# Kernel tuning notes

Hardware: AMD Instinct MI355X
Metric: run time of the kernel (lower is better)

Reference implementation:

```python
import math
import jax, jax.numpy as jnp
import numpy as np
from jax import lax


def _p_n(num_param):
    # Fixed per-kernel sampling grid (torch _get_p_n), row-major over a
    # base_int-wide grid with a partial last row if num_param isn't square.
    base = round(math.sqrt(num_param))
    row = num_param // base
    mod = num_param % base
    xs = np.repeat(np.arange(row), base)
    ys = np.tile(np.arange(base), row)
    if mod > 0:
        xs = np.concatenate([xs, np.full(mod, row)])
        ys = np.concatenate([ys, np.arange(mod)])
    return jnp.asarray(np.concatenate([xs, ys]), jnp.float32)  # [2N]


def _gather_xq(x, q, N):
    # x: [b,c,H,W]; q: [b,h,w,2N] int32 -> [b,c,h,w,N]
    b, c, H, W = x.shape
    h, w = q.shape[1:3]
    idx = q[..., :N] * W + q[..., N:]               # [b,h,w,N]
    xf = x.reshape(b, c, H * W)
    out = jnp.take_along_axis(xf, idx.reshape(b, 1, h * w * N), axis=2)
    return out.reshape(b, c, h, w, N)


def ldconv_forward(x, w_p, b_p, w_conv, num_param, stride):
    b, c, H, W = x.shape
    N = num_param
    dn = ('NCHW', 'OIHW', 'NCHW')
    # offset conv: 3x3, pad 1, stride
    offset = lax.conv_general_dilated(x, w_p, (stride, stride),
                                      [(1, 1), (1, 1)], dimension_numbers=dn)
    offset = offset + b_p[None, :, None, None]      # [b,2N,h,w]
    h, w = offset.shape[2], offset.shape[3]

    p_n = _p_n(N).reshape(1, 2 * N, 1, 1)
    p0x = jnp.broadcast_to((jnp.arange(h, dtype=jnp.float32) * stride)[:, None], (h, w))
    p0y = jnp.broadcast_to((jnp.arange(w, dtype=jnp.float32) * stride)[None, :], (h, w))
    p_0 = jnp.concatenate([jnp.broadcast_to(p0x, (1, N, h, w)),
                           jnp.broadcast_to(p0y, (1, N, h, w))], axis=1)

    p = p_0 + p_n + offset                          # [b,2N,h,w]
    p = jnp.transpose(p, (0, 2, 3, 1))              # [b,h,w,2N]

    q_lt = jnp.floor(lax.stop_gradient(p))
    q_rb = q_lt + 1.0
    clampH = lambda v: jnp.clip(v, 0, H - 1)
    clampW = lambda v: jnp.clip(v, 0, W - 1)
    q_lt = jnp.concatenate([clampH(q_lt[..., :N]), clampW(q_lt[..., N:])], -1).astype(jnp.int32)
    q_rb = jnp.concatenate([clampH(q_rb[..., :N]), clampW(q_rb[..., N:])], -1).astype(jnp.int32)
    q_lb = jnp.concatenate([q_lt[..., :N], q_rb[..., N:]], -1)
    q_rt = jnp.concatenate([q_rb[..., :N], q_lt[..., N:]], -1)

    p = jnp.concatenate([clampH(p[..., :N]), clampW(p[..., N:])], -1)

    px, py = p[..., :N], p[..., N:]
    f = jnp.float32
    g_lt = (1 + (q_lt[..., :N].astype(f) - px)) * (1 + (q_lt[..., N:].astype(f) - py))
    g_rb = (1 - (q_rb[..., :N].astype(f) - px)) * (1 - (q_rb[..., N:].astype(f) - py))
    g_lb = (1 + (q_lb[..., :N].astype(f) - px)) * (1 - (q_lb[..., N:].astype(f) - py))
    g_rt = (1 - (q_rt[..., :N].astype(f) - px)) * (1 + (q_rt[..., N:].astype(f) - py))

    x_q_lt = _gather_xq(x, q_lt, N)
    x_q_rb = _gather_xq(x, q_rb, N)
    x_q_lb = _gather_xq(x, q_lb, N)
    x_q_rt = _gather_xq(x, q_rt, N)

    # [b,c,h,w,N] bilinear blend
    x_offset = (g_lt[:, None] * x_q_lt + g_rb[:, None] * x_q_rb +
                g_lb[:, None] * x_q_lb + g_rt[:, None] * x_q_rt)

    # 'b c h w n -> b c (h n) w'
    x_offset = jnp.transpose(x_offset, (0, 1, 2, 4, 3)).reshape(b, c, h * N, w)

    # final conv: kernel (N,1), stride (N,1), no bias
    out = lax.conv_general_dilated(x_offset, w_conv, (N, 1),
                                   [(0, 0), (0, 0)], dimension_numbers=dn)
    return out


def setup_inputs() -> dict:
    key = jax.random.key(0)
    k1, k2, k3 = jax.random.split(key, 3)
    B, C, H, W = 4, 128, 128, 128
    num_param, outc, stride = 9, 256, 1
    x = jax.random.normal(k1, (B, C, H, W), jnp.float32)
    # small offset-conv weights so sampled offsets stay in a realistic range
    w_p = jax.random.normal(k2, (2 * num_param, C, 3, 3), jnp.float32) * 0.01
    b_p = jnp.zeros((2 * num_param,), jnp.float32)
    w_conv = jax.random.normal(k3, (outc, C, num_param, 1), jnp.float32) * (1.0 / math.sqrt(C * num_param))
    return {"x": x, "w_p": w_p, "b_p": b_p, "w_conv": w_conv,
            "num_param": num_param, "stride": stride}


def reference(x, w_p, b_p, w_conv, num_param, stride):
    return ldconv_forward(x, w_p, b_p, w_conv, num_param, stride)
```

## Files before the change

kernel.cpp:

```cpp
#include <hip/hip_runtime.h>
#include <stdint.h>

#define CIN   128
#define HWSZ  16384
#define NP    9
#define OCH   256
#define KDIM  1152
#define KP    1280

typedef __bf16 bf16_t;
typedef __bf16 bf16x8 __attribute__((ext_vector_type(8)));
typedef float  f32x4  __attribute__((ext_vector_type(4)));
typedef _Float16 f16x4 __attribute__((ext_vector_type(4)));
union MU { uint2 u; f16x4 h; };
struct __attribute__((packed, aligned(4))) F2 { float x, y; };

__device__ __forceinline__ void gll16(const void* g, void* l) {
  __builtin_amdgcn_global_load_lds(
      (const __attribute__((address_space(1))) void*)g,
      (__attribute__((address_space(3))) void*)l, 16, 0, 0);
}

__global__ void k_bt(const float* __restrict__ wc, bf16_t* __restrict__ bt) {
  int k8 = blockIdx.x, og = blockIdx.y, tid = threadIdx.x;
  int i = tid & 7, o = og * 32 + (tid >> 3);
  int kp = k8 * 8 + i;
  int cc = kp / 160, rem = kp % 160;
  int n = rem >> 4, ci = rem & 15;
  int c = cc * 16 + ci;
  float v = (n < 9) ? wc[(o * CIN + c) * NP + n] : 0.f;
  bt[(size_t)k8 * 2048 + o * 8 + i] = (bf16_t)v;
}

__global__ void k_wf(const float* __restrict__ wc, bf16_t* __restrict__ wf) {
  int chunk = blockIdx.x, nf = blockIdx.y, hl = blockIdx.z;
  int lane = threadIdx.x;
  int l15 = lane & 15, quad = lane >> 4;
  int cg = chunk / 9, t = chunk % 9;
  int o = nf * 16 + l15;
  bf16x8 e;
#pragma unroll
  for (int i = 0; i < 8; ++i) {
    int ch = cg * 32 + quad * 8 + i;
    float w = (o < 18) ? wc[((size_t)o * CIN + ch) * NP + t] : 0.f;
    bf16_t h = (bf16_t)w;
    e[i] = hl ? (bf16_t)(w - (float)h) : h;
  }
  *(bf16x8*)((char*)wf + ((((size_t)hl * 36 + chunk) * 2 + nf) * 64 + lane) * 16) = e;
}

__global__ __launch_bounds__(512) void k_off(
    const float* __restrict__ x, const bf16_t* __restrict__ wf,
    const float* __restrict__ bp, int* __restrict__ midx, uint2* __restrict__ mwh)
{
  __shared__ __align__(16) char smem[76032];
  int blk = (blockIdx.x & 7) * 32 + (blockIdx.x >> 3);
  int bb = blk >> 6, ii0 = (blk & 63) << 1;
  int tid = threadIdx.x;
  int wave = tid >> 6, lane = tid & 63;
  int l15 = lane & 15, quad = lane >> 4;

  f32x4 acc[2][2];
#pragma unroll
  for (int f = 0; f < 2; ++f)
#pragma unroll
    for (int nf = 0; nf < 2; ++nf) acc[f][nf] = (f32x4){0.f, 0.f, 0.f, 0.f};

#pragma unroll 1
  for (int cg = 0; cg < 4; ++cg) {
    __syncthreads();
    for (int u = tid; u < 528; u += 512) {
      int row = u / 132, col = u % 132;
      int gr = ii0 - 1 + row, gc = col - 1;
      bool ok = ((unsigned)gr < 128u) && ((unsigned)gc < 128u);
      const float* gp = x + ((size_t)(bb * CIN + cg * 32)) * HWSZ + gr * 128 + gc;
      float v[32];
#pragma unroll
      for (int ch = 0; ch < 32; ++ch) v[ch] = ok ? gp[(size_t)ch * HWSZ] : 0.f;
#pragma unroll
      for (int q8 = 0; q8 < 8; ++q8)
        *(f32x4*)(smem + (size_t)u * 144 + q8 * 16) =
            (f32x4){v[q8 * 4], v[q8 * 4 + 1], v[q8 * 4 + 2], v[q8 * 4 + 3]};
    }
    __syncthreads();
#pragma unroll
    for (int t = 0; t < 9; ++t) {
      int chunk = cg * 9 + t, dy = t / 3, dx = t % 3;
      const char* wb = (const char*)wf;
      bf16x8 bh0 = *(const bf16x8*)(wb + (((size_t)chunk) * 2 + 0) * 1024 + lane * 16);
      bf16x8 bh1 = *(const bf16x8*)(wb + (((size_t)chunk) * 2 + 1) * 1024 + lane * 16);
      bf16x8 bl0 = *(const bf16x8*)(wb + (((size_t)36 + chunk) * 2 + 0) * 1024 + lane * 16);
      bf16x8 bl1 = *(const bf16x8*)(wb + (((size_t)36 + chunk) * 2 + 1) * 1024 + lane * 16);
#pragma unroll
      for (int f = 0; f < 2; ++f) {
        int m = (wave * 2 + f) * 16 + l15;
        int row = (m >> 7) + dy, col = (m & 127) + dx;
        int ent = row * 132 + col;
        f32x4 xlo = *(const f32x4*)(smem + (size_t)ent * 144 + quad * 32);
        f32x4 xhi = *(const f32x4*)(smem + (size_t)ent * 144 + quad * 32 + 16);
        bf16x8 ah, al;
#pragma unroll
        for (int i = 0; i < 4; ++i) {
          float v0 = xlo[i], v1 = xhi[i];
          bf16_t h0 = (bf16_t)v0, h1 = (bf16_t)v1;
          ah[i] = h0; ah[i + 4] = h1;
          al[i] = (bf16_t)(v0 - (float)h0);
          al[i + 4] = (bf16_t)(v1 - (float)h1);
        }
        acc[f][0] = __builtin_amdgcn_mfma_f32_16x16x32_bf16(ah, bh0, acc[f][0], 0, 0, 0);
        acc[f][0] = __builtin_amdgcn_mfma_f32_16x16x32_bf16(ah, bl0, acc[f][0], 0, 0, 0);
        acc[f][0] = __builtin_amdgcn_mfma_f32_16x16x32_bf16(al, bh0, acc[f][0], 0, 0, 0);
        acc[f][1] = __builtin_amdgcn_mfma_f32_16x16x32_bf16(ah, bh1, acc[f][1], 0, 0, 0);
        acc[f][1] = __builtin_amdgcn_mfma_f32_16x16x32_bf16(ah, bl1, acc[f][1], 0, 0, 0);
        acc[f][1] = __builtin_amdgcn_mfma_f32_16x16x32_bf16(al, bh1, acc[f][1], 0, 0, 0);
      }
    }
  }

  __syncthreads();
  float* exch = (float*)smem;
#pragma unroll
  for (int f = 0; f < 2; ++f)
#pragma unroll
    for (int nf = 0; nf < 2; ++nf) {
      int o = nf * 16 + l15;
      if (o < 18) {
#pragma unroll
        for (int r = 0; r < 4; ++r) {
          int pix = (wave * 2 + f) * 16 + quad * 4 + r;
          exch[pix * 20 + o] = acc[f][nf][r];
        }
      }
    }
  __syncthreads();
  if (tid < 256) {
    int pix = tid, iiL = pix >> 7, j = pix & 127, ii = ii0 + iiL;
    float a18[18];
#pragma unroll
    for (int o = 0; o < 18; ++o) a18[o] = exch[pix * 20 + o] + bp[o];
#pragma unroll
    for (int n = 0; n < NP; ++n) {
      float offx = a18[n];
      float offy = a18[9 + n];
      float px = (float)ii + (float)(n / 3) + offx;
      float py = (float)j  + (float)(n % 3) + offy;
      float f0 = floorf(px), f1 = f0 + 1.f;
      float h0 = floorf(py), h1 = h0 + 1.f;
      int r0 = (int)fminf(fmaxf(f0, 0.f), 127.f);
      int r1 = (int)fminf(fmaxf(f1, 0.f), 127.f);
      int c0 = (int)fminf(fmaxf(h0, 0.f), 127.f);
      int c1 = (int)fminf(fmaxf(h1, 0.f), 127.f);
      float pxc = fminf(fmaxf(px, 0.f), 127.f);
      float pyc = fminf(fmaxf(py, 0.f), 127.f);
      float glt = (1.f + ((float)r0 - pxc)) * (1.f + ((float)c0 - pyc));
      float grb = (1.f - ((float)r1 - pxc)) * (1.f - ((float)c1 - pyc));
      float glb = (1.f + ((float)r0 - pxc)) * (1.f - ((float)c1 - pyc));
      float grt = (1.f - ((float)r1 - pxc)) * (1.f + ((float)c0 - pyc));
      int qb = (c0 < 126) ? c0 : 126;
      bool s0 = (c0 != qb), s1 = (c1 != qb);
      float wA = (s0 ? 0.f : glt) + (s1 ? 0.f : glb);
      float wB = (s0 ? glt : 0.f) + (s1 ? glb : 0.f);
      float wC = (s0 ? 0.f : grt) + (s1 ? 0.f : grb);
      float wD = (s0 ? grt : 0.f) + (s1 ? grb : 0.f);
      int base = ((bb * 128 + ii) * NP + n) * 128 + j;
      midx[base] = r0 | (r1 << 8) | (qb << 16);
      MU mu;
      mu.h = (f16x4){(_Float16)wA, (_Float16)wB, (_Float16)wC, (_Float16)wD};
      mwh[base] = mu.u;
    }
  }
}

__global__ __launch_bounds__(512) void k_gg(
    const float* __restrict__ x, const bf16_t* __restrict__ bt,
    const int* __restrict__ midx, const uint2* __restrict__ mwh,
    float* __restrict__ out)
{
  __shared__ __align__(16) char smem[135200];
  char*  Bl    = smem + 74784;
  int*   midxl = (int*)  (smem + 107552);
  uint2* mwhl  = (uint2*)(smem + 116768);

  int blk = (blockIdx.x & 7) * 32 + (blockIdx.x >> 3);
  int bb = blk >> 6, ii0 = (blk & 63) << 1;
  int tid = threadIdx.x;
  int wave = tid >> 6, lane = tid & 63;
  int l15 = lane & 15, quad = lane >> 4;
  int wm = wave >> 2, wo = wave & 3;

  const float* xg = x + (size_t)bb * CIN * HWSZ;

  for (int t = tid; t < 2304; t += 512) {
    int nn = t >> 8, pix = t & 255;
    int iiL = pix >> 7, j = pix & 127;
    int g = ((bb * 128 + ii0 + iiL) * NP + nn) * 128 + j;
    midxl[t] = midx[g];
    mwhl[t]  = mwh[g];
  }

  auto stage_x = [&](int cc) {
    int c0 = cc * 16;
#pragma unroll 2
    for (int k = 0; k < 4; ++k) {
      int e = tid + k * 512;
      int plane = e >> 10;
      int rem = e & 1023;
      int row = rem >> 7, col = rem & 127;
      int r = min(127, max(0, ii0 - 2 + row));
      const float* gp = xg + (size_t)(c0 + plane * 8) * HWSZ + r * 128 + col;
      bf16x8 ev;
#pragma unroll
      for (int i = 0; i < 8; ++i) ev[i] = (bf16_t)gp[(size_t)i * HWSZ];
      *(bf16x8*)(smem + plane * 16912 + (row * 132 + col) * 16) = ev;
    }
  };

  auto gll_B = [&](int stn) {
    const char* src = (const char*)bt + (size_t)stn * 16384 + tid * 16;
    char* dst = Bl + (stn & 1) * 16384 + tid * 16;
    gll16(src, dst);
    gll16(src + 8192, dst + 8192);
  };

  stage_x(0);
  gll_B(0);
  __syncthreads();

  f32x4 acc[8][4];
#pragma unroll
  for (int i = 0; i < 8; ++i)
#pragma unroll
    for (int j2 = 0; j2 < 4; ++j2) acc[i][j2] = (f32x4){0.f, 0.f, 0.f, 0.f};

#pragma unroll 1
  for (int cc = 0; cc < 8; ++cc) {
    if (cc > 0) __syncthreads();
#pragma unroll
    for (int s = 0; s < 5; ++s) {
      int st = cc * 5 + s;
      char* Abuf = smem + 33824 + (st & 1) * 20480;

      int nn = 2 * s + (quad >> 1);
#pragma unroll
      for (int f = 0; f < 2; ++f) {
        int pix = (wave * 2 + f) * 16 + l15;
        bf16x8 av = {};
        if (nn < 9) {
          int im = midxl[nn * 256 + pix];
          MU mu; mu.u = mwhl[nn * 256 + pix];
          float wA = (float)mu.h[0], wB = (float)mu.h[1];
          float wC = (float)mu.h[2], wD = (float)mu.h[3];
          int r0 = im & 255, r1 = (im >> 8) & 255, qb = (im >> 16) & 255;
          int s0 = r0 - ii0 + 2, s1 = r1 - ii0 + 2;
          if (((unsigned)s0 < 8u) & ((unsigned)s1 < 8u)) {
            const char* pb = smem + (quad & 1) * 16912;
            bf16x8 a0 = *(const bf16x8*)(pb + (s0 * 132 + qb) * 16);
            bf16x8 a1 = *(const bf16x8*)(pb + (s0 * 132 + qb) * 16 + 16);
            bf16x8 b0 = *(const bf16x8*)(pb + (s1 * 132 + qb) * 16);
            bf16x8 b1 = *(const bf16x8*)(pb + (s1 * 132 + qb) * 16 + 16);
#pragma unroll
            for (int it = 0; it < 8; ++it)
              av[it] = (bf16_t)(wA * (float)a0[it] + wB * (float)a1[it] +
                                wC * (float)b0[it] + wD * (float)b1[it]);
          } else {
            const float* gb = xg + (size_t)(cc * 16 + (quad & 1) * 8) * HWSZ;
            const float* q0 = gb + r0 * 128 + qb;
            const float* q1 = gb + r1 * 128 + qb;
#pragma unroll
            for (int it = 0; it < 8; ++it) {
              av[it] = (bf16_t)(wA * q0[0] + wB * q0[1] + wC * q1[0] + wD * q1[1]);
              q0 += HWSZ; q1 += HWSZ;
            }
          }
        }
        *(bf16x8*)(Abuf + pix * 80 + quad * 16) = av;
      }

      __syncthreads();
      if (st < 39) gll_B(st + 1);

      {
        const char* Bb = Bl + (st & 1) * 16384;
        bf16x8 bfr[4];
#pragma unroll
        for (int of = 0; of < 4; ++of)
          bfr[of] = *(const bf16x8*)(Bb + quad * 4096 + (wo * 64 + of * 16 + l15) * 16);
#pragma unroll
        for (int mf = 0; mf < 8; ++mf) {
          bf16x8 af = *(const bf16x8*)(Abuf + (wm * 128 + mf * 16 + l15) * 80 + quad * 16);
#pragma unroll
          for (int of = 0; of < 4; ++of)
            acc[mf][of] = __builtin_amdgcn_mfma_f32_16x16x32_bf16(
                af, bfr[of], acc[mf][of], 0, 0, 0);
        }
      }
    }
    if (cc < 7) stage_x(cc + 1);
  }

  __syncthreads();
  float* pw = (float*)smem + wave * 2112;
#pragma unroll
  for (int of = 0; of < 4; ++of) {
#pragma unroll
    for (int mf = 0; mf < 8; ++mf)
      *(f32x4*)(pw + l15 * 132 + mf * 16 + quad * 4) = acc[mf][of];
#pragma unroll
    for (int g = 0; g < 8; ++g) {
      int o_loc = (g & 3) * 4 + quad;
      int mcol = (g >> 2) * 64 + l15 * 4;
      f32x4 v = *(const f32x4*)(pw + o_loc * 132 + mcol);
      int o = wo * 64 + of * 16 + o_loc;
      *(f32x4*)(out + ((size_t)(bb * OCH + o) * 128 + (ii0 + wm)) * 128 + mcol) = v;
    }
  }
}

extern "C" void kernel_launch(void* const* d_in, const int* in_sizes, int n_in,
                              void* d_out, int out_size, void* d_ws, size_t ws_size,
                              hipStream_t stream) {
  const float* x  = (const float*)d_in[0];
  const float* wp = (const float*)d_in[1];
  const float* bp = (const float*)d_in[2];
  const float* wc = (const float*)d_in[3];
  float* out = (float*)d_out;

  bf16_t* BT   = (bf16_t*)d_ws;
  bf16_t* WF   = (bf16_t*)((char*)d_ws + 671744);
  int*    MIDX = (int*)   ((char*)d_ws + (1u << 20));
  uint2*  MWH  = (uint2*) ((char*)d_ws + (4u << 20));

  k_bt<<<dim3(160, 8), 256, 0, stream>>>(wc, BT);
  k_wf<<<dim3(36, 2, 2), 64, 0, stream>>>(wp, WF);
  k_off<<<256, 512, 0, stream>>>(x, WF, bp, MIDX, MWH);
  k_gg<<<256, 512, 0, stream>>>(x, BT, MIDX, MWH, out);
}
```

Before: 192.1 us.

## Halve per-block row tile to one output row, doubling grid for occupancy

Both the offset-conv and the gather-GEMM kernels now process one output row per block instead of two, launching 512 blocks instead of 256. Shared memory shrinks, the halo staging is narrowed, and launch bounds request higher occupancy. The sampling indices and weights are kept in registers instead of being staged through shared memory, and each wave now covers 32 output channels over all 128 pixels. The trade-off is more halo re-reading of x per output row, and the B (weight) tiles are fetched twice as often overall, in exchange for more resident blocks and smaller per-block state.

Result: slower. 251.6 us (+31.0%).

```diff
diff --git a/kernel.cpp b/kernel.cpp
--- a/kernel.cpp
+++ b/kernel.cpp
@@ -5,15 +5,12 @@
 #define HWSZ  16384
 #define NP    9
 #define OCH   256
-#define KDIM  1152
-#define KP    1280
 
 typedef __bf16 bf16_t;
 typedef __bf16 bf16x8 __attribute__((ext_vector_type(8)));
 typedef float  f32x4  __attribute__((ext_vector_type(4)));
 typedef _Float16 f16x4 __attribute__((ext_vector_type(4)));
 union MU { uint2 u; f16x4 h; };
-struct __attribute__((packed, aligned(4))) F2 { float x, y; };
 
 __device__ __forceinline__ void gll16(const void* g, void* l) {
   __builtin_amdgcn_global_load_lds(
@@ -49,29 +46,27 @@
   *(bf16x8*)((char*)wf + ((((size_t)hl * 36 + chunk) * 2 + nf) * 64 + lane) * 16) = e;
 }
 
-__global__ __launch_bounds__(512) void k_off(
+__global__ __launch_bounds__(512, 4) void k_off(
     const float* __restrict__ x, const bf16_t* __restrict__ wf,
     const float* __restrict__ bp, int* __restrict__ midx, uint2* __restrict__ mwh)
 {
-  __shared__ __align__(16) char smem[76032];
-  int blk = (blockIdx.x & 7) * 32 + (blockIdx.x >> 3);
-  int bb = blk >> 6, ii0 = (blk & 63) << 1;
+  __shared__ __align__(16) char smem[57024];
+  int blk = (blockIdx.x & 7) * 64 + (blockIdx.x >> 3);
+  int bb = blk >> 7, ii = blk & 127;
   int tid = threadIdx.x;
   int wave = tid >> 6, lane = tid & 63;
   int l15 = lane & 15, quad = lane >> 4;
 
-  f32x4 acc[2][2];
-#pragma unroll
-  for (int f = 0; f < 2; ++f)
-#pragma unroll
-    for (int nf = 0; nf < 2; ++nf) acc[f][nf] = (f32x4){0.f, 0.f, 0.f, 0.f};
+  f32x4 acc[2];
+  acc[0] = (f32x4){0.f, 0.f, 0.f, 0.f};
+  acc[1] = (f32x4){0.f, 0.f, 0.f, 0.f};
 
 #pragma unroll 1
   for (int cg = 0; cg < 4; ++cg) {
     __syncthreads();
-    for (int u = tid; u < 528; u += 512) {
+    for (int u = tid; u < 396; u += 512) {
       int row = u / 132, col = u % 132;
-      int gr = ii0 - 1 + row, gc = col - 1;
+      int gr = ii - 1 + row, gc = col - 1;
       bool ok = ((unsigned)gr < 128u) && ((unsigned)gc < 128u);
       const float* gp = x + ((size_t)(bb * CIN + cg * 32)) * HWSZ + gr * 128 + gc;
       float v[32];
@@ -91,53 +86,45 @@
       bf16x8 bh1 = *(const bf16x8*)(wb + (((size_t)chunk) * 2 + 1) * 1024 + lane * 16);
       bf16x8 bl0 = *(const bf16x8*)(wb + (((size_t)36 + chunk) * 2 + 0) * 1024 + lane * 16);
       bf16x8 bl1 = *(const bf16x8*)(wb + (((size_t)36 + chunk) * 2 + 1) * 1024 + lane * 16);
-#pragma unroll
-      for (int f = 0; f < 2; ++f) {
-        int m = (wave * 2 + f) * 16 + l15;
-        int row = (m >> 7) + dy, col = (m & 127) + dx;
-        int ent = row * 132 + col;
-        f32x4 xlo = *(const f32x4*)(smem + (size_t)ent * 144 + quad * 32);
-        f32x4 xhi = *(const f32x4*)(smem + (size_t)ent * 144 + quad * 32 + 16);
-        bf16x8 ah, al;
-#pragma unroll
-        for (int i = 0; i < 4; ++i) {
-          float v0 = xlo[i], v1 = xhi[i];
-          bf16_t h0 = (bf16_t)v0, h1 = (bf16_t)v1;
-          ah[i] = h0; ah[i + 4] = h1;
-          al[i] = (bf16_t)(v0 - (float)h0);
-          al[i + 4] = (bf16_t)(v1 - (float)h1);
-        }
-        acc[f][0] = __builtin_amdgcn_mfma_f32_16x16x32_bf16(ah, bh0, acc[f][0], 0, 0, 0);
-        acc[f][0] = __builtin_amdgcn_mfma_f32_16x16x32_bf16(ah, bl0, acc[f][0], 0, 0, 0);
-        acc[f][0] = __builtin_amdgcn_mfma_f32_16x16x32_bf16(al, bh0, acc[f][0], 0, 0, 0);
-        acc[f][1] = __builtin_amdgcn_mfma_f32_16x16x32_bf16(ah, bh1, acc[f][1], 0, 0, 0);
-        acc[f][1] = __builtin_amdgcn_mfma_f32_16x16x32_bf16(ah, bl1, acc[f][1], 0, 0, 0);
-        acc[f][1] = __builtin_amdgcn_mfma_f32_16x16x32_bf16(al, bh1, acc[f][1], 0, 0, 0);
+      int m = wave * 16 + l15;
+      int ent = dy * 132 + m + dx;
+      f32x4 xlo = *(const f32x4*)(smem + (size_t)ent * 144 + quad * 32);
+      f32x4 xhi = *(const f32x4*)(smem + (size_t)ent * 144 + quad * 32 + 16);
+      bf16x8 ah, al;
+#pragma unroll
+      for (int i = 0; i < 4; ++i) {
+        float v0 = xlo[i], v1 = xhi[i];
+        bf16_t h0 = (bf16_t)v0, h1 = (bf16_t)v1;
+        ah[i] = h0; ah[i + 4] = h1;
+        al[i] = (bf16_t)(v0 - (float)h0);
+        al[i + 4] = (bf16_t)(v1 - (float)h1);
       }
+      acc[0] = __builtin_amdgcn_mfma_f32_16x16x32_bf16(ah, bh0, acc[0], 0, 0, 0);
+      acc[0] = __builtin_amdgcn_mfma_f32_16x16x32_bf16(ah, bl0, acc[0], 0, 0, 0);
+      acc[0] = __builtin_amdgcn_mfma_f32_16x16x32_bf16(al, bh0, acc[0], 0, 0, 0);
+      acc[1] = __builtin_amdgcn_mfma_f32_16x16x32_bf16(ah, bh1, acc[1], 0, 0, 0);
+      acc[1] = __builtin_amdgcn_mfma_f32_16x16x32_bf16(ah, bl1, acc[1], 0, 0, 0);
+      acc[1] = __builtin_amdgcn_mfma_f32_16x16x32_bf16(al, bh1, acc[1], 0, 0, 0);
     }
   }
 
   __syncthreads();
   float* exch = (float*)smem;
 #pragma unroll
-  for (int f = 0; f < 2; ++f)
-#pragma unroll
-    for (int nf = 0; nf < 2; ++nf) {
-      int o = nf * 16 + l15;
-      if (o < 18) {
-#pragma unroll
-        for (int r = 0; r < 4; ++r) {
-          int pix = (wave * 2 + f) * 16 + quad * 4 + r;
-          exch[pix * 20 + o] = acc[f][nf][r];
-        }
-      }
-    }
+  for (int nf = 0; nf < 2; ++nf) {
+    int o = nf * 16 + l15;
+    if (o < 18) {
+#pragma unroll
+      for (int r = 0; r < 4; ++r)
+        exch[(wave * 16 + quad * 4 + r) * 20 + o] = acc[nf][r];
+    }
+  }
   __syncthreads();
-  if (tid < 256) {
-    int pix = tid, iiL = pix >> 7, j = pix & 127, ii = ii0 + iiL;
+  if (tid < 128) {
+    int j = tid;
     float a18[18];
 #pragma unroll
-    for (int o = 0; o < 18; ++o) a18[o] = exch[pix * 20 + o] + bp[o];
+    for (int o = 0; o < 18; ++o) a18[o] = exch[j * 20 + o] + bp[o];
 #pragma unroll
     for (int n = 0; n < NP; ++n) {
       float offx = a18[n];
@@ -171,31 +158,40 @@
   }
 }
 
-__global__ __launch_bounds__(512) void k_gg(
+__global__ __launch_bounds__(512, 4) void k_gg(
     const float* __restrict__ x, const bf16_t* __restrict__ bt,
     const int* __restrict__ midx, const uint2* __restrict__ mwh,
     float* __restrict__ out)
 {
-  __shared__ __align__(16) char smem[135200];
-  char*  Bl    = smem + 74784;
-  int*   midxl = (int*)  (smem + 107552);
-  uint2* mwhl  = (uint2*)(smem + 116768);
-
-  int blk = (blockIdx.x & 7) * 32 + (blockIdx.x >> 3);
-  int bb = blk >> 6, ii0 = (blk & 63) << 1;
+  __shared__ __align__(16) char smem[81920];
+  char* XP = smem;
+  char* Al = smem + 32768;
+  char* Bl = smem + 49152;
+
+  int blk = (blockIdx.x & 7) * 64 + (blockIdx.x >> 3);
+  int bb = blk >> 7, ii = blk & 127;
   int tid = threadIdx.x;
   int wave = tid >> 6, lane = tid & 63;
   int l15 = lane & 15, quad = lane >> 4;
-  int wm = wave >> 2, wo = wave & 3;
+  int pix = tid & 127;
+  int qq  = tid >> 7;
+  int nh = qq >> 1, plane = qq & 1;
 
   const float* xg = x + (size_t)bb * CIN * HWSZ;
 
-  for (int t = tid; t < 2304; t += 512) {
-    int nn = t >> 8, pix = t & 255;
-    int iiL = pix >> 7, j = pix & 127;
-    int g = ((bb * 128 + ii0 + iiL) * NP + nn) * 128 + j;
-    midxl[t] = midx[g];
-    mwhl[t]  = mwh[g];
+  int   pmi[5];
+  uint2 pmw[5];
+#pragma unroll
+  for (int s = 0; s < 5; ++s) {
+    int n = 2 * s + nh;
+    if (n < 9) {
+      int g = ((bb * 128 + ii) * NP + n) * 128 + pix;
+      pmi[s] = midx[g];
+      pmw[s] = mwh[g];
+    } else {
+      pmi[s] = -1;
+      pmw[s] = make_uint2(0u, 0u);
+    }
   }
 
   auto stage_x = [&](int cc) {
@@ -203,15 +199,15 @@
 #pragma unroll 2
     for (int k = 0; k < 4; ++k) {
       int e = tid + k * 512;
-      int plane = e >> 10;
+      int pl = e >> 10;
       int rem = e & 1023;
       int row = rem >> 7, col = rem & 127;
-      int r = min(127, max(0, ii0 - 2 + row));
-      const float* gp = xg + (size_t)(c0 + plane * 8) * HWSZ + r * 128 + col;
+      int r = min(127, max(0, ii - 2 + row));
+      const float* gp = xg + (size_t)(c0 + pl * 8) * HWSZ + r * 128 + col;
       bf16x8 ev;
 #pragma unroll
       for (int i = 0; i < 8; ++i) ev[i] = (bf16_t)gp[(size_t)i * HWSZ];
-      *(bf16x8*)(smem + plane * 16912 + (row * 132 + col) * 16) = ev;
+      *(bf16x8*)(XP + pl * 16384 + (row * 128 + col) * 16) = ev;
     }
   };
 
@@ -224,13 +220,14 @@
 
   stage_x(0);
   gll_B(0);
+
+  f32x4 acc[8][2];
+#pragma unroll
+  for (int i = 0; i < 8; ++i)
+#pragma unroll
+    for (int j2 = 0; j2 < 2; ++j2) acc[i][j2] = (f32x4){0.f, 0.f, 0.f, 0.f};
+
   __syncthreads();
-
-  f32x4 acc[8][4];
-#pragma unroll
-  for (int i = 0; i < 8; ++i)
-#pragma unroll
-    for (int j2 = 0; j2 < 4; ++j2) acc[i][j2] = (f32x4){0.f, 0.f, 0.f, 0.f};
 
 #pragma unroll 1
   for (int cc = 0; cc < 8; ++cc) {
@@ -238,32 +235,29 @@
 #pragma unroll
     for (int s = 0; s < 5; ++s) {
       int st = cc * 5 + s;
-      char* Abuf = smem + 33824 + (st & 1) * 20480;
-
-      int nn = 2 * s + (quad >> 1);
-#pragma unroll
-      for (int f = 0; f < 2; ++f) {
-        int pix = (wave * 2 + f) * 16 + l15;
+      char* Abuf = Al + (st & 1) * 8192;
+
+      {
         bf16x8 av = {};
-        if (nn < 9) {
-          int im = midxl[nn * 256 + pix];
-          MU mu; mu.u = mwhl[nn * 256 + pix];
+        int im = pmi[s];
+        if (im >= 0) {
+          MU mu; mu.u = pmw[s];
           float wA = (float)mu.h[0], wB = (float)mu.h[1];
           float wC = (float)mu.h[2], wD = (float)mu.h[3];
           int r0 = im & 255, r1 = (im >> 8) & 255, qb = (im >> 16) & 255;
-          int s0 = r0 - ii0 + 2, s1 = r1 - ii0 + 2;
+          int s0 = r0 - ii + 2, s1 = r1 - ii + 2;
           if (((unsigned)s0 < 8u) & ((unsigned)s1 < 8u)) {
-            const char* pb = smem + (quad & 1) * 16912;
-            bf16x8 a0 = *(const bf16x8*)(pb + (s0 * 132 + qb) * 16);
-            bf16x8 a1 = *(const bf16x8*)(pb + (s0 * 132 + qb) * 16 + 16);
-            bf16x8 b0 = *(const bf16x8*)(pb + (s1 * 132 + qb) * 16);
-            bf16x8 b1 = *(const bf16x8*)(pb + (s1 * 132 + qb) * 16 + 16);
+            const char* pb = XP + plane * 16384;
+            bf16x8 a0 = *(const bf16x8*)(pb + (s0 * 128 + qb) * 16);
+            bf16x8 a1 = *(const bf16x8*)(pb + (s0 * 128 + qb + 1) * 16);
+            bf16x8 b0 = *(const bf16x8*)(pb + (s1 * 128 + qb) * 16);
+            bf16x8 b1 = *(const bf16x8*)(pb + (s1 * 128 + qb + 1) * 16);
 #pragma unroll
             for (int it = 0; it < 8; ++it)
               av[it] = (bf16_t)(wA * (float)a0[it] + wB * (float)a1[it] +
                                 wC * (float)b0[it] + wD * (float)b1[it]);
           } else {
-            const float* gb = xg + (size_t)(cc * 16 + (quad & 1) * 8) * HWSZ;
+            const float* gb = xg + (size_t)(cc * 16 + plane * 8) * HWSZ;
             const float* q0 = gb + r0 * 128 + qb;
             const float* q1 = gb + r1 * 128 + qb;
 #pragma unroll
@@ -273,7 +267,7 @@
             }
           }
         }
-        *(bf16x8*)(Abuf + pix * 80 + quad * 16) = av;
+        *(bf16x8*)(Abuf + (qq * 128 + pix) * 16) = av;
       }
 
       __syncthreads();
@@ -281,15 +275,15 @@
 
       {
         const char* Bb = Bl + (st & 1) * 16384;
-        bf16x8 bfr[4];
-#pragma unroll
-        for (int of = 0; of < 4; ++of)
-          bfr[of] = *(const bf16x8*)(Bb + quad * 4096 + (wo * 64 + of * 16 + l15) * 16);
+        bf16x8 bfr[2];
+#pragma unroll
+        for (int of = 0; of < 2; ++of)
+          bfr[of] = *(const bf16x8*)(Bb + quad * 4096 + (wave * 32 + of * 16 + l15) * 16);
 #pragma unroll
         for (int mf = 0; mf < 8; ++mf) {
-          bf16x8 af = *(const bf16x8*)(Abuf + (wm * 128 + mf * 16 + l15) * 80 + quad * 16);
-#pragma unroll
-          for (int of = 0; of < 4; ++of)
+          bf16x8 af = *(const bf16x8*)(Abuf + (quad * 128 + mf * 16 + l15) * 16);
+#pragma unroll
+          for (int of = 0; of < 2; ++of)
             acc[mf][of] = __builtin_amdgcn_mfma_f32_16x16x32_bf16(
                 af, bfr[of], acc[mf][of], 0, 0, 0);
         }
@@ -301,7 +295,7 @@
   __syncthreads();
   float* pw = (float*)smem + wave * 2112;
 #pragma unroll
-  for (int of = 0; of < 4; ++of) {
+  for (int of = 0; of < 2; ++of) {
 #pragma unroll
     for (int mf = 0; mf < 8; ++mf)
       *(f32x4*)(pw + l15 * 132 + mf * 16 + quad * 4) = acc[mf][of];
@@ -310,8 +304,8 @@
       int o_loc = (g & 3) * 4 + quad;
       int mcol = (g >> 2) * 64 + l15 * 4;
       f32x4 v = *(const f32x4*)(pw + o_loc * 132 + mcol);
-      int o = wo * 64 + of * 16 + o_loc;
-      *(f32x4*)(out + ((size_t)(bb * OCH + o) * 128 + (ii0 + wm)) * 128 + mcol) = v;
+      int o = wave * 32 + of * 16 + o_loc;
+      *(f32x4*)(out + ((size_t)(bb * OCH + o) * 128 + ii) * 128 + mcol) = v;
     }
   }
 }
@@ -332,6 +326,6 @@
 
   k_bt<<<dim3(160, 8), 256, 0, stream>>>(wc, BT);
   k_wf<<<dim3(36, 2, 2), 64, 0, stream>>>(wp, WF);
-  k_off<<<256, 512, 0, stream>>>(x, WF, bp, MIDX, MWH);
-  k_gg<<<256, 512, 0, stream>>>(x, BT, MIDX, MWH, out);
-}
+  k_off<<<512, 512, 0, stream>>>(x, WF, bp, MIDX, MWH);
+  k_gg<<<512, 512, 0, stream>>>(x, BT, MIDX, MWH, out);
+}
```
